# Kernel tuning notes

Hardware: AMD Instinct MI355X
Metric: run time of the kernel (lower is better)

Reference implementation:

```python
import jax, jax.numpy as jnp
import numpy as np

N = 100_000      # nodes
E = 1_600_000    # edges (avg degree 16)
F_IN, H1, H2, C = 128, 256, 64, 40


def gcn_conv(x, W, b, src, dst, n):
    """PyG GCNConv with self-loops already appended to (src, dst).
    out[i] = sum_{(j->i)} d_j^-1/2 d_i^-1/2 (x W)[j] + b, d = in-degree incl. self-loop."""
    xw = x @ W  # [n, out_dim]
    deg = jax.ops.segment_sum(jnp.ones(src.shape[0], x.dtype), dst, num_segments=n)
    dinv = jnp.where(deg > 0, jax.lax.rsqrt(deg), jnp.zeros((), x.dtype))
    norm = dinv[src] * dinv[dst]  # [E+N]
    out = jax.ops.segment_sum(xw[src] * norm[:, None], dst, num_segments=n)
    return out + b


def setup_inputs() -> dict:
    key = jax.random.key(0)
    ks = jax.random.split(key, 5)
    x = jax.random.normal(ks[0], (N, F_IN), dtype=jnp.float32)
    edge_index = jax.random.randint(ks[1], (2, E), 0, N, dtype=jnp.int64)
    W1 = jax.random.normal(ks[2], (F_IN, H1), dtype=jnp.float32) * (1.0 / np.sqrt(F_IN))
    b1 = jnp.zeros((H1,), jnp.float32)
    W2 = jax.random.normal(ks[3], (H1, H2), dtype=jnp.float32) * (1.0 / np.sqrt(H1))
    b2 = jnp.zeros((H2,), jnp.float32)
    Wfc = jax.random.normal(ks[4], (H2, C), dtype=jnp.float32) * (1.0 / np.sqrt(H2))
    bfc = jnp.zeros((C,), jnp.float32)
    return {"x": x, "edge_index": edge_index, "W1": W1, "b1": b1,
            "W2": W2, "b2": b2, "Wfc": Wfc, "bfc": bfc}


def reference(x, edge_index, W1, b1, W2, b2, Wfc, bfc):
    n = x.shape[0]
    # add self-loops (fixed shape, jit-friendly)
    loops = jnp.arange(n, dtype=edge_index.dtype)
    src = jnp.concatenate([edge_index[0], loops])
    dst = jnp.concatenate([edge_index[1], loops])
    h = gcn_conv(x, W1, b1, src, dst, n)
    h = jax.nn.relu(h)
    h = gcn_conv(h, W2, b2, src, dst, n)
    return h @ Wfc + bfc
```

## Files before the change

### kernel.cpp

```cpp
#include <hip/hip_runtime.h>

#define N_NODES 100000
#define N_EDGES 1600000
#define NBUCK   3125
#define NGRP    8
#define GCAP    128

typedef __attribute__((ext_vector_type(8))) _Float16 half8_t;
typedef __attribute__((ext_vector_type(4))) float f32x4_t;
typedef __attribute__((ext_vector_type(4))) _Float16 half4_t;
typedef __attribute__((ext_vector_type(2))) _Float16 half2_t;

static __device__ __forceinline__ int2 nt_load_i2(const int2* p) {
    long long raw = __builtin_nontemporal_load((const long long*)p);
    return make_int2((int)(unsigned)(raw & 0xffffffffll), (int)(raw >> 32));
}

__global__ void bcur_init_kernel(int* __restrict__ bcur, int nc) {
    int i = blockIdx.x * blockDim.x + threadIdx.x;
    if (i < nc) bcur[i] = i * GCAP;
}

__global__ void bucket_kernel(const int* __restrict__ src, const int* __restrict__ dst,
                              int* __restrict__ bcur, int2* __restrict__ tmp, int E) {
    int i = blockIdx.x * blockDim.x + threadIdx.x;
    if (i >= E) return;
    unsigned xcc;
    asm volatile("s_getreg_b32 %0, hwreg(HW_REG_XCC_ID)" : "=s"(xcc));
    int g = (int)(xcc & (NGRP - 1));
    int s = __builtin_nontemporal_load(&src[i]);
    int d = __builtin_nontemporal_load(&dst[i]);
    int pos = atomicAdd(&bcur[(d >> 5) * NGRP + g], 1);
    tmp[pos] = make_int2(s, d);
}

__global__ __launch_bounds__(256) void bdeg_kernel(const int* __restrict__ bcur,
                                                   const int2* __restrict__ tmp,
                                                   int* __restrict__ deg, int n) {
    __shared__ int ld[32];
    int b = blockIdx.x, t = threadIdx.x;
    if (t < 32) ld[t] = 0;
    __syncthreads();
    for (int g = 0; g < NGRP; ++g) {
        int base = (b * NGRP + g) * GCAP;
        int e1 = bcur[b * NGRP + g];
        for (int e = base + t; e < e1; e += 256) {
            int2 p = nt_load_i2(&tmp[e]);
            atomicAdd(&ld[p.y & 31], 1);
        }
    }
    __syncthreads();
    int node = b * 32 + t;
    if (t < 32 && node < n) deg[node] = ld[t];
}

__global__ __launch_bounds__(256) void place_kernel(const int* __restrict__ bcur,
                                                    const int2* __restrict__ tmp,
                                                    const int* __restrict__ rowptr,
                                                    const float* __restrict__ dinv,
                                                    int2* __restrict__ csr, int n) {
    __shared__ int lc[32];
    int b = blockIdx.x, t = threadIdx.x;
    if (t < 32) lc[t] = 0;
    __syncthreads();
    for (int g = 0; g < NGRP; ++g) {
        int base = (b * NGRP + g) * GCAP;
        int e1 = bcur[b * NGRP + g];
        for (int e = base + t; e < e1; e += 256) {
            int2 p = nt_load_i2(&tmp[e]);
            int pos = atomicAdd(&lc[p.y & 31], 1);
            float w = dinv[p.x] * dinv[p.y];
            csr[rowptr[p.y] + pos] = make_int2(p.x, __float_as_int(w));
        }
    }
}

__global__ void dinv_kernel(const int* __restrict__ deg, float* __restrict__ dinv, int n) {
    int i = blockIdx.x * blockDim.x + threadIdx.x;
    if (i < n) dinv[i] = rsqrtf((float)(deg[i] + 1));
}

__global__ void scan_sums_kernel(const int* __restrict__ deg, int* __restrict__ bsums, int n) {
    __shared__ int sd[256];
    int t = threadIdx.x;
    int base = blockIdx.x * 1024 + t * 4;
    int s = 0;
    #pragma unroll
    for (int j = 0; j < 4; ++j) { int i = base + j; if (i < n) s += deg[i]; }
    sd[t] = s; __syncthreads();
    for (int off = 128; off > 0; off >>= 1) {
        if (t < off) sd[t] += sd[t + off];
        __syncthreads();
    }
    if (t == 0) bsums[blockIdx.x] = sd[0];
}

__global__ void scan_offsets_kernel(int* __restrict__ bsums, int nb, int* __restrict__ rowptr_tail) {
    __shared__ int sd[128];
    int t = threadIdx.x;
    int v = (t < nb) ? bsums[t] : 0;
    sd[t] = v; __syncthreads();
    for (int off = 1; off < 128; off <<= 1) {
        int x = (t >= off) ? sd[t - off] : 0;
        __syncthreads();
        sd[t] += x;
        __syncthreads();
    }
    if (t < nb) bsums[t] = sd[t] - v;
    if (t == 0) *rowptr_tail = N_EDGES;
}

__global__ void scan_final_kernel(const int* __restrict__ deg, const int* __restrict__ bsums,
                                  int* __restrict__ rowptr, int n) {
    __shared__ int sd[256];
    int t = threadIdx.x;
    int base = blockIdx.x * 1024 + t * 4;
    int v[4], pre[4], s = 0;
    #pragma unroll
    for (int j = 0; j < 4; ++j) {
        int i = base + j;
        v[j] = (i < n) ? deg[i] : 0;
        pre[j] = s; s += v[j];
    }
    sd[t] = s;
    int mine = s;
    __syncthreads();
    for (int off = 1; off < 256; off <<= 1) {
        int x = (t >= off) ? sd[t - off] : 0;
        __syncthreads();
        sd[t] += x;
        __syncthreads();
    }
    int excl = sd[t] - mine + bsums[blockIdx.x];
    #pragma unroll
    for (int j = 0; j < 4; ++j) {
        int i = base + j;
        if (i < n) rowptr[i] = excl + pre[j];
    }
}

__global__ void x16_kernel(const float* __restrict__ x, _Float16* __restrict__ y, int total4) {
    int i = blockIdx.x * blockDim.x + threadIdx.x;
    if (i >= total4) return;
    float4 v = *(const float4*)&x[(size_t)i * 4];
    half4_t o;
    o[0] = (_Float16)v.x; o[1] = (_Float16)v.y;
    o[2] = (_Float16)v.z; o[3] = (_Float16)v.w;
    *(half4_t*)&y[(size_t)i * 4] = o;
}

__global__ __launch_bounds__(256) void w2fc_kernel(
        const float* __restrict__ W2, const float* __restrict__ Wfc,
        const float* __restrict__ b2, const float* __restrict__ bfc,
        _Float16* __restrict__ T16, float* __restrict__ bfc2) {
    __shared__ float wf[64 * 40];
    int t = threadIdx.x;
    for (int i = t; i < 64 * 40; i += 256) wf[i] = Wfc[i];
    __syncthreads();
    float acc[40];
    #pragma unroll
    for (int c = 0; c < 40; ++c) acc[c] = 0.f;
    for (int k = 0; k < 64; ++k) {
        float a = W2[t * 64 + k];
        #pragma unroll
        for (int c = 0; c < 40; ++c) acc[c] += a * wf[k * 40 + c];
    }
    #pragma unroll
    for (int c = 0; c < 40; ++c) T16[c * 256 + t] = (_Float16)acc[c];
    #pragma unroll
    for (int r = 40; r < 48; ++r) T16[r * 256 + t] = (_Float16)0.f;
    if (t < 40) {
        float s = bfc[t];
        for (int k = 0; k < 64; ++k) s += b2[k] * wf[k * 40 + t];
        bfc2[t] = s;
    }
}

__global__ void w1t_kernel(const float* __restrict__ W1, _Float16* __restrict__ t16) {
    int k = blockIdx.x;
    int n = threadIdx.x;
    t16[n * 128 + k] = (_Float16)W1[k * 256 + n];
}

__global__ void gather1_kernel(const int* __restrict__ rowptr, const int2* __restrict__ csr,
                               const float* __restrict__ dinv, const _Float16* __restrict__ x,
                               _Float16* __restrict__ o16, int n) {
    const int lane = threadIdx.x & 63;
    const int wid0 = (blockIdx.x * blockDim.x + threadIdx.x) >> 6;
    const int nwav = (gridDim.x * blockDim.x) >> 6;
    for (int node = wid0; node < n; node += nwav) {
        float di = dinv[node];
        float selfw = di * di;
        int e0 = rowptr[node], e1 = rowptr[node + 1];
        const half2_t sv = *(const half2_t*)&x[(size_t)node * 128 + lane * 2];
        float ax = (float)sv[0] * selfw, ay = (float)sv[1] * selfw;
        int e = e0;
        for (; e + 8 <= e1; e += 8) {
            int2 p[8]; half2_t v[8];
            #pragma unroll
            for (int u = 0; u < 8; ++u) p[u] = nt_load_i2(&csr[e + u]);
            #pragma unroll
            for (int u = 0; u < 8; ++u)
                v[u] = *(const half2_t*)&x[(size_t)p[u].x * 128 + lane * 2];
            #pragma unroll
            for (int u = 0; u < 8; ++u) {
                float w = __int_as_float(p[u].y);
                ax += (float)v[u][0] * w; ay += (float)v[u][1] * w;
            }
        }
        for (; e + 4 <= e1; e += 4) {
            int2 p[4]; half2_t v[4];
            #pragma unroll
            for (int u = 0; u < 4; ++u) p[u] = nt_load_i2(&csr[e + u]);
            #pragma unroll
            for (int u = 0; u < 4; ++u)
                v[u] = *(const half2_t*)&x[(size_t)p[u].x * 128 + lane * 2];
            #pragma unroll
            for (int u = 0; u < 4; ++u) {
                float w = __int_as_float(p[u].y);
                ax += (float)v[u][0] * w; ay += (float)v[u][1] * w;
            }
        }
        for (; e < e1; ++e) {
            int2 p = nt_load_i2(&csr[e]);
            float w = __int_as_float(p.y);
            const half2_t v = *(const half2_t*)&x[(size_t)p.x * 128 + lane * 2];
            ax += (float)v[0] * w; ay += (float)v[1] * w;
        }
        half2_t ov; ov[0] = (_Float16)ax; ov[1] = (_Float16)ay;
        *(half2_t*)&o16[(size_t)node * 128 + lane * 2] = ov;
    }
}

__global__ void gather2_kernel(const int* __restrict__ rowptr, const int2* __restrict__ csr,
                               const float* __restrict__ dinv, const float* __restrict__ xw,
                               const float* __restrict__ bias, float* __restrict__ out, int n) {
    const int lane = threadIdx.x & 63;
    const int wid0 = (blockIdx.x * blockDim.x + threadIdx.x) >> 6;
    const int nwav = (gridDim.x * blockDim.x) >> 6;
    const int cl = lane < 40 ? lane : 39;
    for (int node = wid0; node < n; node += nwav) {
        float di = dinv[node];
        float selfw = di * di;
        int e0 = rowptr[node], e1 = rowptr[node + 1];
        float acc = xw[(size_t)node * 40 + cl] * selfw;
        int e = e0;
        for (; e + 8 <= e1; e += 8) {
            int2 p[8]; float v[8];
            #pragma unroll
            for (int u = 0; u < 8; ++u) p[u] = nt_load_i2(&csr[e + u]);
            #pragma unroll
            for (int u = 0; u < 8; ++u) v[u] = xw[(size_t)p[u].x * 40 + cl];
            #pragma unroll
            for (int u = 0; u < 8; ++u) acc += v[u] * __int_as_float(p[u].y);
        }
        for (; e < e1; ++e) {
            int2 p = nt_load_i2(&csr[e]);
            acc += xw[(size_t)p.x * 40 + cl] * __int_as_float(p.y);
        }
        acc += bias[cl];
        if (lane < 40) out[(size_t)node * 40 + lane] = acc;
    }
}

__global__ __launch_bounds__(256) void gemm1_mfma(
        const _Float16* __restrict__ A16, const _Float16* __restrict__ B16,
        const float* __restrict__ bias, _Float16* __restrict__ C16, int M) {
    constexpr int K = 128, N = 256, LDK = 40;
    __shared__ _Float16 sA[128 * LDK];
    __shared__ _Float16 sB[128 * LDK];
    const int t = threadIdx.x;
    const int m0 = blockIdx.x * 128, n0 = blockIdx.y * 128;
    const int wave = t >> 6, lane = t & 63;
    const int wm = wave >> 1, wn = wave & 1;
    const int l15 = lane & 15, k8 = (lane >> 4) * 8;

    f32x4_t acc[4][4] = {};

    for (int k0 = 0; k0 < K; k0 += 32) {
        #pragma unroll
        for (int u = 0; u < 2; ++u) {
            int idx = t + u * 256;
            int r = idx >> 2, c = (idx & 3) * 8;
            int gr = m0 + r; if (gr > M - 1) gr = M - 1;
            *(uint4*)&sA[r * LDK + c] = *(const uint4*)&A16[(size_t)gr * K + k0 + c];
            int bn = n0 + r;
            *(uint4*)&sB[r * LDK + c] = *(const uint4*)&B16[(size_t)bn * K + k0 + c];
        }
        __syncthreads();
        half8_t fa[4], fb[4];
        #pragma unroll
        for (int i = 0; i < 4; ++i) {
            int m = wm * 64 + i * 16 + l15;
            fa[i] = *(const half8_t*)&sA[m * LDK + k8];
            int nn = wn * 64 + i * 16 + l15;
            fb[i] = *(const half8_t*)&sB[nn * LDK + k8];
        }
        #pragma unroll
        for (int i = 0; i < 4; ++i)
            #pragma unroll
            for (int j = 0; j < 4; ++j)
                acc[i][j] = __builtin_amdgcn_mfma_f32_16x16x32_f16(fa[i], fb[j], acc[i][j], 0, 0, 0);
        __syncthreads();
    }

    const int r4 = (lane >> 4) * 4;
    #pragma unroll
    for (int j = 0; j < 4; ++j) {
        int col = n0 + wn * 64 + j * 16 + l15;
        float bv = bias[col];
        #pragma unroll
        for (int i = 0; i < 4; ++i) {
            #pragma unroll
            for (int r = 0; r < 4; ++r) {
                int row = m0 + wm * 64 + i * 16 + r4 + r;
                if (row < M) {
                    float v = fmaxf(acc[i][j][r] + bv, 0.f);
                    C16[(size_t)row * N + col] = (_Float16)v;
                }
            }
        }
    }
}

__global__ __launch_bounds__(256) void gemm2_mfma(
        const _Float16* __restrict__ A16, const _Float16* __restrict__ B16,
        float* __restrict__ C, int M) {
    constexpr int K = 256, LDK = 40;
    __shared__ _Float16 sA[128 * LDK];
    __shared__ _Float16 sB[48 * LDK];
    const int t = threadIdx.x;
    const int m0 = blockIdx.x * 128;
    const int wave = t >> 6, lane = t & 63;
    const int l15 = lane & 15, k8 = (lane >> 4) * 8;

    f32x4_t acc[2][3] = {};

    for (int k0 = 0; k0 < K; k0 += 32) {
        #pragma unroll
        for (int u = 0; u < 2; ++u) {
            int idx = t + u * 256;
            int r = idx >> 2, c = (idx & 3) * 8;
            int gr = m0 + r; if (gr > M - 1) gr = M - 1;
            *(uint4*)&sA[r * LDK + c] = *(const uint4*)&A16[(size_t)gr * K + k0 + c];
        }
        if (t < 192) {
            int r = t >> 2, c = (t & 3) * 8;
            *(uint4*)&sB[r * LDK + c] = *(const uint4*)&B16[(size_t)r * K + k0 + c];
        }
        __syncthreads();
        half8_t fa[2], fb[3];
        #pragma unroll
        for (int i = 0; i < 2; ++i) {
            int m = wave * 32 + i * 16 + l15;
            fa[i] = *(const half8_t*)&sA[m * LDK + k8];
        }
        #pragma unroll
        for (int j = 0; j < 3; ++j) {
            int nn = j * 16 + l15;
            fb[j] = *(const half8_t*)&sB[nn * LDK + k8];
        }
        #pragma unroll
        for (int i = 0; i < 2; ++i)
            #pragma unroll
            for (int j = 0; j < 3; ++j)
                acc[i][j] = __builtin_amdgcn_mfma_f32_16x16x32_f16(fa[i], fb[j], acc[i][j], 0, 0, 0);
        __syncthreads();
    }

    const int r4 = (lane >> 4) * 4;
    #pragma unroll
    for (int i = 0; i < 2; ++i)
        #pragma unroll
        for (int j = 0; j < 3; ++j) {
            int col = j * 16 + l15;
            if (col < 40) {
                #pragma unroll
                for (int r = 0; r < 4; ++r) {
                    int row = m0 + wave * 32 + i * 16 + r4 + r;
                    if (row < M) C[(size_t)row * 40 + col] = acc[i][j][r];
                }
            }
        }
}

extern "C" void kernel_launch(void* const* d_in, const int* in_sizes, int n_in,
                              void* d_out, int out_size, void* d_ws, size_t ws_size,
                              hipStream_t stream) {
    const float* x   = (const float*)d_in[0];
    const int*   ei  = (const int*)d_in[1];
    const float* W1  = (const float*)d_in[2];
    const float* b1  = (const float*)d_in[3];
    const float* W2  = (const float*)d_in[4];
    const float* b2  = (const float*)d_in[5];
    const float* Wfc = (const float*)d_in[6];
    const float* bfc = (const float*)d_in[7];
    float* out = (float*)d_out;

    const int n = N_NODES, E = N_EDGES;
    const int* src = ei;
    const int* dst = ei + E;

    char* ws = (char*)d_ws;
    int*       deg    = (int*)(ws + 0);
    float*     dinv   = (float*)(ws + 409600);
    int*       rowptr = (int*)(ws + 819200);
    int*       bsums  = (int*)(ws + 1219584);
    float*     bfc2   = (float*)(ws + 1220096);
    _Float16*  w2t16  = (_Float16*)(ws + 1220608);
    _Float16*  w1t16  = (_Float16*)(ws + 1245184);
    int*       bcur   = (int*)(ws + 1310720);
    int2*      csr    = (int2*)(ws + 1413120);
    int2*      tmp    = (int2*)(ws + 14213120);
    _Float16*  x16    = (_Float16*)(ws + 39813120);
    _Float16*  aggx16 = (_Float16*)(ws + 65413120);
    _Float16*  h116   = (_Float16*)(ws + 91013120);
    float*     h1w    = (float*)(ws + 142213120);

    const int nb = (n + 1023) / 1024;

    bcur_init_kernel<<<(NBUCK * NGRP + 255) / 256, 256, 0, stream>>>(bcur, NBUCK * NGRP);
    bucket_kernel<<<(E + 255) / 256, 256, 0, stream>>>(src, dst, bcur, tmp, E);
    bdeg_kernel<<<NBUCK, 256, 0, stream>>>(bcur, tmp, deg, n);
    dinv_kernel<<<(n + 255) / 256, 256, 0, stream>>>(deg, dinv, n);
    scan_sums_kernel<<<nb, 256, 0, stream>>>(deg, bsums, n);
    scan_offsets_kernel<<<1, 128, 0, stream>>>(bsums, nb, rowptr + n);
    scan_final_kernel<<<nb, 256, 0, stream>>>(deg, bsums, rowptr, n);
    place_kernel<<<NBUCK, 256, 0, stream>>>(bcur, tmp, rowptr, dinv, csr, n);

    w2fc_kernel<<<1, 256, 0, stream>>>(W2, Wfc, b2, bfc, w2t16, bfc2);
    w1t_kernel<<<128, 256, 0, stream>>>(W1, w1t16);
    x16_kernel<<<(n * 128 / 4 + 255) / 256, 256, 0, stream>>>(x, x16, n * 32);

    gather1_kernel<<<2048, 256, 0, stream>>>(rowptr, csr, dinv, x16, aggx16, n);
    gemm1_mfma<<<dim3((n + 127) / 128, 2), 256, 0, stream>>>(
        aggx16, w1t16, b1, h116, n);

    gemm2_mfma<<<(n + 127) / 128, 256, 0, stream>>>(h116, w2t16, h1w, n);
    gather2_kernel<<<2048, 256, 0, stream>>>(rowptr, csr, dinv, h1w, bfc2, out, n);
}
```

Before: 354.5 us.

## Replace atomic bucket scatter with two-pass counting sort into 1024-node bins

Replaces per-edge global atomic bucketing into fixed-capacity 32-node buckets with a histogram pass, a bin prefix scan, and a block-local LDS-staged counting sort that writes edges contiguously per 1024-node bin. Degree counting and CSR placement then run one 1024-thread block per bin. This cuts global atomic traffic and padded temp storage and makes the scatter writes more coalesced. In exchange it reads dst one extra time and leaves only 98 blocks for the degree and place kernels, which limits parallelism.

```diff
diff --git a/kernel.cpp b/kernel.cpp
--- a/kernel.cpp
+++ b/kernel.cpp
@@ -2,9 +2,8 @@
 
 #define N_NODES 100000
 #define N_EDGES 1600000
-#define NBUCK   3125
-#define NGRP    8
-#define GCAP    128
+#define NBIN    98
+#define CHUNK   4096
 
 typedef __attribute__((ext_vector_type(8))) _Float16 half8_t;
 typedef __attribute__((ext_vector_type(4))) float f32x4_t;
@@ -16,62 +15,120 @@
     return make_int2((int)(unsigned)(raw & 0xffffffffll), (int)(raw >> 32));
 }
 
-__global__ void bcur_init_kernel(int* __restrict__ bcur, int nc) {
-    int i = blockIdx.x * blockDim.x + threadIdx.x;
-    if (i < nc) bcur[i] = i * GCAP;
-}
-
-__global__ void bucket_kernel(const int* __restrict__ src, const int* __restrict__ dst,
-                              int* __restrict__ bcur, int2* __restrict__ tmp, int E) {
-    int i = blockIdx.x * blockDim.x + threadIdx.x;
-    if (i >= E) return;
-    unsigned xcc;
-    asm volatile("s_getreg_b32 %0, hwreg(HW_REG_XCC_ID)" : "=s"(xcc));
-    int g = (int)(xcc & (NGRP - 1));
-    int s = __builtin_nontemporal_load(&src[i]);
-    int d = __builtin_nontemporal_load(&dst[i]);
-    int pos = atomicAdd(&bcur[(d >> 5) * NGRP + g], 1);
-    tmp[pos] = make_int2(s, d);
-}
-
-__global__ __launch_bounds__(256) void bdeg_kernel(const int* __restrict__ bcur,
-                                                   const int2* __restrict__ tmp,
-                                                   int* __restrict__ deg, int n) {
-    __shared__ int ld[32];
+__global__ __launch_bounds__(256) void hist_kernel(const int* __restrict__ dst,
+                                                   int* __restrict__ bhist, int E) {
+    __shared__ int lh[NBIN];
+    int t = threadIdx.x;
+    for (int i = t; i < NBIN; i += 256) lh[i] = 0;
+    __syncthreads();
+    int base = blockIdx.x * CHUNK;
+    int end = base + CHUNK; if (end > E) end = E;
+    for (int i = base + t; i < end; i += 256)
+        atomicAdd(&lh[__builtin_nontemporal_load(&dst[i]) >> 10], 1);
+    __syncthreads();
+    for (int i = t; i < NBIN; i += 256)
+        if (lh[i]) atomicAdd(&bhist[i], lh[i]);
+}
+
+__global__ void binscan_kernel(const int* __restrict__ bhist,
+                               int* __restrict__ bbase, int* __restrict__ gcur) {
+    __shared__ int sd[128];
+    int t = threadIdx.x;
+    int v = (t < NBIN) ? bhist[t] : 0;
+    sd[t] = v; __syncthreads();
+    for (int off = 1; off < 128; off <<= 1) {
+        int x = (t >= off) ? sd[t - off] : 0;
+        __syncthreads();
+        sd[t] += x;
+        __syncthreads();
+    }
+    if (t < NBIN) { bbase[t] = sd[t] - v; gcur[t] = sd[t] - v; }
+}
+
+__global__ __launch_bounds__(256) void binning_kernel(
+        const int* __restrict__ src, const int* __restrict__ dst,
+        int* __restrict__ gcur, int2* __restrict__ tmp, int E) {
+    __shared__ int lh[NBIN];
+    __shared__ int lbase[NBIN];
+    __shared__ int gbase[NBIN];
+    __shared__ int sc[128];
+    __shared__ int2 stage[CHUNK];
+    __shared__ unsigned char binid[CHUNK];
+    int t = threadIdx.x;
+    int base = blockIdx.x * CHUNK;
+    int end = base + CHUNK; if (end > E) end = E;
+
+    for (int i = t; i < NBIN; i += 256) lh[i] = 0;
+    __syncthreads();
+    for (int i = base + t; i < end; i += 256)
+        atomicAdd(&lh[__builtin_nontemporal_load(&dst[i]) >> 10], 1);
+    __syncthreads();
+    if (t < 128) sc[t] = (t < NBIN) ? lh[t] : 0;
+    __syncthreads();
+    for (int off = 1; off < 128; off <<= 1) {
+        int x = 0;
+        if (t < 128 && t >= off) x = sc[t - off];
+        __syncthreads();
+        if (t < 128) sc[t] += x;
+        __syncthreads();
+    }
+    if (t < NBIN) {
+        int cnt = lh[t];
+        lbase[t] = sc[t] - cnt;
+        gbase[t] = cnt ? atomicAdd(&gcur[t], cnt) : 0;
+        lh[t] = 0;
+    }
+    __syncthreads();
+    for (int i = base + t; i < end; i += 256) {
+        int s = __builtin_nontemporal_load(&src[i]);
+        int d = __builtin_nontemporal_load(&dst[i]);
+        int b = d >> 10;
+        int lp = lbase[b] + atomicAdd(&lh[b], 1);
+        stage[lp] = make_int2(s, d);
+        binid[lp] = (unsigned char)b;
+    }
+    __syncthreads();
+    int tot = end - base;
+    for (int i = t; i < tot; i += 256) {
+        int b = binid[i];
+        tmp[gbase[b] + (i - lbase[b])] = stage[i];
+    }
+}
+
+__global__ __launch_bounds__(1024) void bdeg_kernel(const int* __restrict__ bbase,
+                                                    const int* __restrict__ bhist,
+                                                    const int2* __restrict__ tmp,
+                                                    int* __restrict__ deg, int n) {
+    __shared__ int ld[1024];
     int b = blockIdx.x, t = threadIdx.x;
-    if (t < 32) ld[t] = 0;
-    __syncthreads();
-    for (int g = 0; g < NGRP; ++g) {
-        int base = (b * NGRP + g) * GCAP;
-        int e1 = bcur[b * NGRP + g];
-        for (int e = base + t; e < e1; e += 256) {
-            int2 p = nt_load_i2(&tmp[e]);
-            atomicAdd(&ld[p.y & 31], 1);
-        }
-    }
-    __syncthreads();
-    int node = b * 32 + t;
-    if (t < 32 && node < n) deg[node] = ld[t];
-}
-
-__global__ __launch_bounds__(256) void place_kernel(const int* __restrict__ bcur,
-                                                    const int2* __restrict__ tmp,
-                                                    const int* __restrict__ rowptr,
-                                                    const float* __restrict__ dinv,
-                                                    int2* __restrict__ csr, int n) {
-    __shared__ int lc[32];
+    ld[t] = 0;
+    __syncthreads();
+    int e0 = bbase[b], e1 = e0 + bhist[b];
+    for (int e = e0 + t; e < e1; e += 1024) {
+        int2 p = nt_load_i2(&tmp[e]);
+        atomicAdd(&ld[p.y & 1023], 1);
+    }
+    __syncthreads();
+    int node = b * 1024 + t;
+    if (node < n) deg[node] = ld[t];
+}
+
+__global__ __launch_bounds__(1024) void place_kernel(const int* __restrict__ bbase,
+                                                     const int* __restrict__ bhist,
+                                                     const int2* __restrict__ tmp,
+                                                     const int* __restrict__ rowptr,
+                                                     const float* __restrict__ dinv,
+                                                     int2* __restrict__ csr, int n) {
+    __shared__ int lc[1024];
     int b = blockIdx.x, t = threadIdx.x;
-    if (t < 32) lc[t] = 0;
-    __syncthreads();
-    for (int g = 0; g < NGRP; ++g) {
-        int base = (b * NGRP + g) * GCAP;
-        int e1 = bcur[b * NGRP + g];
-        for (int e = base + t; e < e1; e += 256) {
-            int2 p = nt_load_i2(&tmp[e]);
-            int pos = atomicAdd(&lc[p.y & 31], 1);
-            float w = dinv[p.x] * dinv[p.y];
-            csr[rowptr[p.y] + pos] = make_int2(p.x, __float_as_int(w));
-        }
+    lc[t] = 0;
+    __syncthreads();
+    int e0 = bbase[b], e1 = e0 + bhist[b];
+    for (int e = e0 + t; e < e1; e += 1024) {
+        int2 p = nt_load_i2(&tmp[e]);
+        int pos = atomicAdd(&lc[p.y & 1023], 1);
+        float w = dinv[p.x] * dinv[p.y];
+        csr[rowptr[p.y] + pos] = make_int2(p.x, __float_as_int(w));
     }
 }
 
@@ -409,24 +466,29 @@
     float*     bfc2   = (float*)(ws + 1220096);
     _Float16*  w2t16  = (_Float16*)(ws + 1220608);
     _Float16*  w1t16  = (_Float16*)(ws + 1245184);
-    int*       bcur   = (int*)(ws + 1310720);
-    int2*      csr    = (int2*)(ws + 1413120);
-    int2*      tmp    = (int2*)(ws + 14213120);
-    _Float16*  x16    = (_Float16*)(ws + 39813120);
-    _Float16*  aggx16 = (_Float16*)(ws + 65413120);
-    _Float16*  h116   = (_Float16*)(ws + 91013120);
-    float*     h1w    = (float*)(ws + 142213120);
+    int*       bhist  = (int*)(ws + 1310720);
+    int*       bbase  = (int*)(ws + 1311232);
+    int*       gcur   = (int*)(ws + 1311744);
+    int2*      csr    = (int2*)(ws + 1312768);
+    int2*      tmp    = (int2*)(ws + 14112768);
+    _Float16*  x16    = (_Float16*)(ws + 26912768);
+    _Float16*  aggx16 = (_Float16*)(ws + 52512768);
+    _Float16*  h116   = (_Float16*)(ws + 78112768);
+    float*     h1w    = (float*)(ws + 129312768);
 
     const int nb = (n + 1023) / 1024;
-
-    bcur_init_kernel<<<(NBUCK * NGRP + 255) / 256, 256, 0, stream>>>(bcur, NBUCK * NGRP);
-    bucket_kernel<<<(E + 255) / 256, 256, 0, stream>>>(src, dst, bcur, tmp, E);
-    bdeg_kernel<<<NBUCK, 256, 0, stream>>>(bcur, tmp, deg, n);
+    const int nchunk = (E + CHUNK - 1) / CHUNK;
+
+    hipMemsetAsync(bhist, 0, 512, stream);
+    hist_kernel<<<nchunk, 256, 0, stream>>>(dst, bhist, E);
+    binscan_kernel<<<1, 128, 0, stream>>>(bhist, bbase, gcur);
+    binning_kernel<<<nchunk, 256, 0, stream>>>(src, dst, gcur, tmp, E);
+    bdeg_kernel<<<NBIN, 1024, 0, stream>>>(bbase, bhist, tmp, deg, n);
     dinv_kernel<<<(n + 255) / 256, 256, 0, stream>>>(deg, dinv, n);
     scan_sums_kernel<<<nb, 256, 0, stream>>>(deg, bsums, n);
     scan_offsets_kernel<<<1, 128, 0, stream>>>(bsums, nb, rowptr + n);
     scan_final_kernel<<<nb, 256, 0, stream>>>(deg, bsums, rowptr, n);
-    place_kernel<<<NBUCK, 256, 0, stream>>>(bcur, tmp, rowptr, dinv, csr, n);
+    place_kernel<<<NBIN, 1024, 0, stream>>>(bbase, bhist, tmp, rowptr, dinv, csr, n);
 
     w2fc_kernel<<<1, 256, 0, stream>>>(W2, Wfc, b2, bfc, w2t16, bfc2);
     w1t_kernel<<<128, 256, 0, stream>>>(W1, w1t16);
```

Result: no change. 357.3 us (+0.8%).
